# Kernel optimization log

Measured on AMD Instinct MI355X. Metric: run time of the kernel, lower is better.

## Reference

```python
import jax, jax.numpy as jnp
import numpy as np

EPS = 1.1920929e-07  # torch F.rms_norm default eps for fp32
D, NH, NKV, HD = 1024, 16, 4, 64
MLP_MULT, L = 3, 6           # L = num_layers // 2 shared blocks
VS, HS, LS, ROPE_B = 50257, 4096, 30.0, 10000.0
B, S = 2, 2048


def rmsn(x):
    return x * jax.lax.rsqrt(jnp.mean(jnp.square(x), -1, keepdims=True) + EPS)


def rope_tables(s):
    f = 1.0 / ROPE_B ** (jnp.arange(0, HD, 2, dtype=jnp.float32) / HD)
    fr = jnp.outer(jnp.arange(s, dtype=jnp.float32), f)  # [s, HD/2]
    return jnp.cos(fr), jnp.sin(fr)


def rot(x, c, s):
    h = x.shape[-1] // 2
    x1, x2 = x[..., :h], x[..., h:]
    return jnp.concatenate([x1 * c + x2 * s, -x1 * s + x2 * c], -1)


def attn(x, Wq, Wk, Wv, Wo, qg, cos, sin):
    b, s, d = x.shape
    q = (x @ Wq.T).reshape(b, s, NH, HD).swapaxes(1, 2)    # [b,nh,s,hd]
    k = (x @ Wk.T).reshape(b, s, NKV, HD).swapaxes(1, 2)   # [b,nkv,s,hd]
    v = (x @ Wv.T).reshape(b, s, NKV, HD).swapaxes(1, 2)
    q, k = rmsn(q), rmsn(k)                                # QK RMSNorm (no weight)
    c, si = cos[None, None], sin[None, None]
    q, k = rot(q, c, si), rot(k, c, si)
    q = q * qg[None, :, None, None]                        # per-head gate
    g = NH // NKV
    qr = q.reshape(b, NKV, g, s, HD)
    scores = jnp.einsum('bkgqd,bksd->bkgqs', qr, k) / jnp.sqrt(jnp.float32(HD))
    mask = jnp.tril(jnp.ones((s, s), bool))
    scores = jnp.where(mask, scores, -jnp.inf)
    p = jax.nn.softmax(scores, -1)
    y = jnp.einsum('bkgqs,bksd->bkgqd', p, v).reshape(b, NH, s, HD)
    y = y.swapaxes(1, 2).reshape(b, s, d)
    return y @ Wo.T


def mlp(x, Wf, Wo2):
    return jnp.square(jax.nn.relu(x @ Wf.T)) @ Wo2.T       # ReLU^2 MLP


def block(x, x0, p, cos, sin):
    Wq, Wk, Wv, Wo, qg, a_sc, m_sc, rm, Wf, Wo2 = p
    x = rm[0] * x + rm[1] * x0                             # learned residual mix
    x = x + a_sc * attn(rmsn(x), Wq, Wk, Wv, Wo, qg, cos, sin)
    x = x + m_sc * mlp(rmsn(x), Wf, Wo2)
    return x


def setup_inputs() -> dict:
    key = jax.random.key(0)
    ks = jax.random.split(key, 16)
    sd = 0.02
    return {
        'ids': jax.random.randint(ks[0], (B, S), 0, VS, dtype=jnp.int32),
        'y': jax.random.randint(ks[1], (B, S), 0, VS, dtype=jnp.int32),
        'u_emb': jax.random.normal(ks[2], (VS, D // 2), jnp.float32) * 0.02,
        'b_emb': jax.random.normal(ks[3], (HS, D // 2), jnp.float32) * 0.01,
        'Wq': jax.random.normal(ks[4], (L, D, D), jnp.float32) * sd,
        'Wk': jax.random.normal(ks[5], (L, NKV * HD, D), jnp.float32) * sd,
        'Wv': jax.random.normal(ks[6], (L, NKV * HD, D), jnp.float32) * sd,
        'Wo': jax.random.normal(ks[7], (L, D, D), jnp.float32) * sd,
        'qg': jnp.ones((L, NH), jnp.float32),
        'a_scale': jnp.ones((L, D), jnp.float32),
        'm_scale': jnp.ones((L, D), jnp.float32),
        'rm': jnp.stack([jnp.full((L, D), 0.7, jnp.float32), jnp.full((L, D), 0.3, jnp.float32)], 1),
        'Wf': jax.random.normal(ks[8], (L, MLP_MULT * D, D), jnp.float32) * sd,
        'Wo2': jax.random.normal(ks[9], (L, D, MLP_MULT * D), jnp.float32) * sd,
        'sw': jnp.ones((L, D), jnp.float32),
    }


def reference(ids, y, u_emb, b_emb, Wq, Wk, Wv, Wo, qg, a_scale, m_scale, rm, Wf, Wo2, sw):
    b, s = ids.shape
    # BigramHash embedding: (prev_id*VS + id) % HS, computed mod-HS to stay in int32
    pi = jnp.pad(ids[:, :-1], ((0, 0), (1, 0)))
    bi = (((pi % HS) * (VS % HS)) % HS + ids % HS) % HS
    h = jnp.concatenate([u_emb[ids], b_emb[bi]], -1)       # [b,s,D]
    h = rmsn(h)
    cos, sin = rope_tables(s)
    h0, sk = h, []
    for i in range(L):                                     # encoder half
        p = (Wq[i], Wk[i], Wv[i], Wo[i], qg[i], a_scale[i], m_scale[i], rm[i], Wf[i], Wo2[i])
        h = block(h, h0, p, cos, sin)
        sk.append(h)
    for i in range(L):                                     # decoder half (reversed blocks, skips)
        h = h + sw[i] * sk[L - 1 - i]
        j = L - 1 - i
        p = (Wq[j], Wk[j], Wv[j], Wo[j], qg[j], a_scale[j], m_scale[j], rm[j], Wf[j], Wo2[j])
        h = block(h, h0, p, cos, sin)
    h = rmsn(h)
    # tied bigram-hash head: out_weight = [u_emb | zeros]  ->  only first D/2 dims matter
    lg = h.reshape(-1, D)[:, :D // 2] @ u_emb.T            # [b*s, VS]
    lg = LS * jnp.tanh(lg / LS)                            # logit softcap
    logp = jax.nn.log_softmax(lg.astype(jnp.float32), -1)
    yf = y.reshape(-1)
    loss = -jnp.mean(jnp.take_along_axis(logp, yf[:, None], 1)[:, 0])
    return loss
```

## Files before the change

### kernel.cpp

```cpp
#include <hip/hip_runtime.h>
#include <cstdint>
#include <cstddef>

constexpr int   Dm    = 1024;
constexpr int   NHn   = 16;
constexpr int   NKVn  = 4;
constexpr int   HDn   = 64;
constexpr int   Ln    = 6;
constexpr int   Sn    = 2048;
constexpr int   Bn    = 2;
constexpr int   ROWS  = Bn * Sn;
constexpr int   VSn   = 50257;
constexpr int   HSn   = 4096;
constexpr float EPSF  = 1.1920929e-07f;
constexpr int   VCHUNK = 4096;
constexpr int   VPAD   = 50304;
constexpr float LOG2E  = 1.44269504f;

#define DEV __device__ __forceinline__

typedef __attribute__((ext_vector_type(8))) short bf16x8;
typedef __attribute__((ext_vector_type(4))) float f32x4;
using ush = unsigned short;

DEV ush f2bf(float f) {
    unsigned int u = __float_as_uint(f);
    u = (u + 0x7fffu + ((u >> 16) & 1u)) >> 16;
    return (ush)u;
}

DEV float b2f(ush v) {
    return __uint_as_float(((unsigned int)v) << 16);
}

DEV f32x4 mfma16(bf16x8 a, bf16x8 b, f32x4 c) {
    return __builtin_amdgcn_mfma_f32_16x16x32_bf16(a, b, c, 0, 0, 0);
}

DEV void llds16(const ush* g, ush* l) {
    __builtin_amdgcn_global_load_lds(
        (const __attribute__((address_space(1))) void*)g,
        (__attribute__((address_space(3))) void*)l, 16, 0, 0);
}

DEV float block_sum256(float v, float* red) {
#pragma unroll
    for (int off = 32; off; off >>= 1) v += __shfl_xor(v, off);
    __syncthreads();
    if ((threadIdx.x & 63) == 0) red[threadIdx.x >> 6] = v;
    __syncthreads();
    return red[0] + red[1] + red[2] + red[3];
}

DEV float block_max256(float v, float* red) {
#pragma unroll
    for (int off = 32; off; off >>= 1) v = fmaxf(v, __shfl_xor(v, off));
    __syncthreads();
    if ((threadIdx.x & 63) == 0) red[threadIdx.x >> 6] = v;
    __syncthreads();
    return fmaxf(fmaxf(red[0], red[1]), fmaxf(red[2], red[3]));
}

__global__ void rope_kernel(float* __restrict__ cb, float* __restrict__ sb) {
    int idx = blockIdx.x * 256 + threadIdx.x;
    if (idx >= Sn * 32) return;
    int t = idx >> 5, f = idx & 31;
    float freq = powf(10000.f, -(float)f * (1.f / 32.f));
    float ang  = (float)t * freq;
    cb[idx] = cosf(ang);
    sb[idx] = sinf(ang);
}

__global__ void cvt_bf16_kernel(const float* __restrict__ s, ush* __restrict__ d, int n4) {
    int i = blockIdx.x * 256 + threadIdx.x;
    if (i >= n4) return;
    float4 v = *(const float4*)(s + (size_t)i * 4);
    ushort4 o;
    o.x = f2bf(v.x); o.y = f2bf(v.y); o.z = f2bf(v.z); o.w = f2bf(v.w);
    *(ushort4*)(d + (size_t)i * 4) = o;
}

__global__ void zpad_kernel(ush* __restrict__ p, int n) {
    int i = blockIdx.x * 256 + threadIdx.x;
    if (i < n) p[i] = 0;
}

__global__ __launch_bounds__(256)
void embed_kernel(const int* __restrict__ ids, const float* __restrict__ ue,
                  const float* __restrict__ be, float* __restrict__ h,
                  float* __restrict__ h0) {
    __shared__ float red[4];
    int r = blockIdx.x;
    int s = r % Sn;
    int id = ids[r];
    int prev = (s == 0) ? 0 : ids[r - 1];
    int bi = ((prev % HSn) * (VSn % HSn) % HSn + id % HSn) % HSn;
    int tid = threadIdx.x;
    float vals[4];
    float ss = 0.f;
#pragma unroll
    for (int t = 0; t < 4; ++t) {
        int j = tid + t * 256;
        float v = (j < 512) ? ue[(size_t)id * 512 + j]
                            : be[(size_t)bi * 512 + (j - 512)];
        vals[t] = v; ss += v * v;
    }
    ss = block_sum256(ss, red);
    float rinv = rsqrtf(ss * (1.f / Dm) + EPSF);
#pragma unroll
    for (int t = 0; t < 4; ++t) {
        int j = tid + t * 256;
        float v = vals[t] * rinv;
        h [(size_t)r * Dm + j] = v;
        h0[(size_t)r * Dm + j] = v;
    }
}

__global__ __launch_bounds__(256)
void resmix_kernel(float* __restrict__ h, const float* __restrict__ h0,
                   const float* __restrict__ rm0, ush* __restrict__ xnb) {
    __shared__ float red[4];
    int r = blockIdx.x, tid = threadIdx.x;
    const float* rm1 = rm0 + Dm;
    float vals[4]; float ss = 0.f;
#pragma unroll
    for (int t = 0; t < 4; ++t) {
        int j = tid + t * 256;
        size_t o = (size_t)r * Dm + j;
        float v = rm0[j] * h[o] + rm1[j] * h0[o];
        vals[t] = v; ss += v * v;
        h[o] = v;
    }
    ss = block_sum256(ss, red);
    float rinv = rsqrtf(ss * (1.f / Dm) + EPSF);
#pragma unroll
    for (int t = 0; t < 4; ++t)
        xnb[(size_t)r * Dm + tid + t * 256] = f2bf(vals[t] * rinv);
}

__global__ __launch_bounds__(256)
void rmsn_kernel(const float* __restrict__ x, ush* __restrict__ out) {
    __shared__ float red[4];
    int r = blockIdx.x, tid = threadIdx.x;
    float vals[4]; float ss = 0.f;
#pragma unroll
    for (int t = 0; t < 4; ++t) {
        float v = x[(size_t)r * Dm + tid + t * 256];
        vals[t] = v; ss += v * v;
    }
    ss = block_sum256(ss, red);
    float rinv = rsqrtf(ss * (1.f / Dm) + EPSF);
#pragma unroll
    for (int t = 0; t < 4; ++t)
        out[(size_t)r * Dm + tid + t * 256] = f2bf(vals[t] * rinv);
}

__global__ __launch_bounds__(256)
void skipadd_kernel(float* __restrict__ h, const ush* __restrict__ skb,
                    const float* __restrict__ sc) {
    int r = blockIdx.x, tid = threadIdx.x;
#pragma unroll
    for (int t = 0; t < 4; ++t) {
        int j = tid + t * 256;
        size_t o = (size_t)r * Dm + j;
        h[o] = fmaf(sc[j], b2f(skb[o]), h[o]);
    }
}

template<int TM, int MODE>
__global__ __launch_bounds__(256)
void gemm_k(const ush* __restrict__ A, const ush* __restrict__ B,
            ush* __restrict__ C, int M, int N, int K,
            int lda, int ldb, int ldc,
            float* __restrict__ hres, const float* __restrict__ sc,
            ush* __restrict__ dup) {
    __shared__ __align__(16) ush As[TM * 32];
    __shared__ __align__(16) ush Bs[128 * 32];
    const int m0 = blockIdx.x * TM, n0 = blockIdx.y * 128;
    const int tid  = threadIdx.x;
    const int w    = tid >> 6, lane = tid & 63;
    const int l15  = lane & 15, quad = lane >> 4;
    const int wr   = w >> 1, wc = w & 1;
    constexpr int NI = TM / 32;

    const int srow = lane >> 2, sch = lane & 3;
    const ush* Ag;
    ush* AsW;
    if constexpr (TM == 128) {
        Ag  = A + (size_t)(m0 + w * 32 + srow) * lda + sch * 8;
        AsW = As + w * 1024;
    } else {
        Ag  = A + (size_t)(m0 + w * 16 + srow) * lda + sch * 8;
        AsW = As + w * 512;
    }
    const ush* Bg = B + (size_t)(n0 + w * 32 + srow) * ldb + sch * 8;
    ush* BsW = Bs + w * 1024;

    f32x4 acc[NI][4] = {};

    for (int k0 = 0; k0 < K; k0 += 32) {
        __syncthreads();
        llds16(Ag + k0, AsW);
        if constexpr (TM == 128) llds16(Ag + k0 + 16 * lda, AsW + 512);
        llds16(Bg + k0,            BsW);
        llds16(Bg + k0 + 16 * ldb, BsW + 512);
        __syncthreads();
        bf16x8 af[NI], bfv[4];
#pragma unroll
        for (int i = 0; i < NI; ++i)
            af[i] = *(const bf16x8*)&As[(wr * (TM / 2) + i * 16 + l15) * 32 + quad * 8];
#pragma unroll
        for (int j = 0; j < 4; ++j)
            bfv[j] = *(const bf16x8*)&Bs[(wc * 64 + j * 16 + l15) * 32 + quad * 8];
#pragma unroll
        for (int i = 0; i < NI; ++i)
#pragma unroll
            for (int j = 0; j < 4; ++j)
                acc[i][j] = mfma16(af[i], bfv[j], acc[i][j]);
    }

#pragma unroll
    for (int i = 0; i < NI; ++i) {
#pragma unroll
        for (int j = 0; j < 4; ++j) {
            int row = m0 + wr * (TM / 2) + i * 16 + quad * 4;
            int col = n0 + wc * 64 + j * 16 + l15;
#pragma unroll
            for (int r = 0; r < 4; ++r) {
                float v = acc[i][j][r];
                if (MODE == 1) { v = fmaxf(v, 0.f); v = v * v; }
                else if (MODE == 2) {
                    float ax = fabsf(v) * (1.f / 30.f);
                    float e  = __expf(-2.f * ax);
                    float t  = (1.f - e) / (1.f + e);
                    v = copysignf(t * 30.f, v);
                }
                if (MODE == 3) {
                    size_t o = (size_t)(row + r) * ldc + col;
                    float nv = fmaf(sc[col], v, hres[o]);
                    hres[o] = nv;
                    if (dup) dup[o] = f2bf(nv);
                } else {
                    C[(size_t)(row + r) * ldc + col] = f2bf(v);
                }
            }
        }
    }
}

__global__ __launch_bounds__(256)
void qknorm_rope_kernel(const ush* __restrict__ in,
                        ush* __restrict__ qout, ush* __restrict__ kout,
                        const float* __restrict__ cosb, const float* __restrict__ sinb,
                        const float* __restrict__ qg) {
    int idx  = blockIdx.x * 4 + (threadIdx.x >> 6);
    int lane = threadIdx.x & 63;
    int t, hh, in_off;
    ush* outp; int out_ld;
    bool isq = idx < ROWS * NHn;
    if (isq) { t = idx >> 4; hh = idx & 15; in_off = hh * 64; outp = qout; out_ld = 1024; }
    else { int i2 = idx - ROWS * NHn; t = i2 >> 2; hh = i2 & 3; in_off = 1024 + hh * 64; outp = kout; out_ld = 256; }
    int sidx = t % Sn;
    float x = b2f(in[(size_t)t * 1536 + in_off + lane]);
    float ss = x * x;
#pragma unroll
    for (int off = 32; off; off >>= 1) ss += __shfl_xor(ss, off);
    float xn = x * rsqrtf(ss * (1.f / HDn) + EPSF);
    float partner = __shfl_xor(xn, 32);
    int f = lane & 31;
    float c  = cosb[sidx * 32 + f];
    float sv = sinb[sidx * 32 + f];
    float o = (lane < 32) ? fmaf(xn, c, partner * sv)
                          : fmaf(xn, c, -partner * sv);
    if (isq) o *= qg[hh] * (0.125f * LOG2E);
    outp[(size_t)t * out_ld + hh * 64 + lane] = f2bf(o);
}

__global__ __launch_bounds__(256)
void vtrans_kernel(const ush* __restrict__ in, ush* __restrict__ out) {
    __shared__ ush tile[32][33];
    int s0 = blockIdx.x * 32;
    int c0 = blockIdx.y * 32;
    int i = threadIdx.x >> 5;
    int j = threadIdx.x & 31;
#pragma unroll
    for (int k = 0; k < 4; ++k)
        tile[i + k * 8][j] = in[(size_t)(s0 + i + k * 8) * 1536 + 1280 + c0 + j];
    __syncthreads();
#pragma unroll
    for (int k = 0; k < 4; ++k)
        out[(size_t)(c0 + i + k * 8) * (size_t)ROWS + s0 + j] = tile[j][i + k * 8];
}

__global__ __launch_bounds__(256)
void attn_mfma_kernel(const ush* __restrict__ qb,
                      const ush* __restrict__ kb,
                      const ush* __restrict__ vt,
                      ush* __restrict__ ob,
                      const float* __restrict__ qgl) {
    __shared__ __align__(16) ush Ks[64 * 72];
    __shared__ __align__(16) ush Vs[64 * 72];
    __shared__ __align__(16) unsigned int PsD[128 * 36];
    const int tile = 15 - (blockIdx.x & 15);
    const int h    = (blockIdx.x >> 4) & 15;
    const int b    = blockIdx.x >> 8;
    const int kvh  = h >> 2;
    const int w    = threadIdx.x >> 6, lane = threadIdx.x & 63;
    const int l15  = lane & 15, quad = lane >> 4;
    const int q0   = tile * 128;
    const float mfix = 8.f * fabsf(qgl[h]) * LOG2E;

    bf16x8 qf[2][2];
    {
        size_t qr = (size_t)(b * Sn + q0 + w * 32 + l15) * 1024 + h * 64;
        qf[0][0] = *(const bf16x8*)(qb + qr + quad * 8);
        qf[0][1] = *(const bf16x8*)(qb + qr + 32 + quad * 8);
        qf[1][0] = *(const bf16x8*)(qb + qr + 16 * 1024 + quad * 8);
        qf[1][1] = *(const bf16x8*)(qb + qr + 16 * 1024 + 32 + quad * 8);
    }
    f32x4 Oacc[2][4] = {};
    float lsum[2][4] = {{0.f,0.f,0.f,0.f},{0.f,0.f,0.f,0.f}};

    const int rrS = threadIdx.x >> 3, chS = threadIdx.x & 7;
    const size_t kbase = (size_t)(b * Sn) * 256 + kvh * 64;
    const size_t vbase = (size_t)(kvh * 64) * (size_t)ROWS + b * Sn;
    const int nblk = 2 * tile + 2;

    uint4 kr0 = *(const uint4*)(kb + kbase + (size_t)rrS * 256 + chS * 8);
    uint4 kr1 = *(const uint4*)(kb + kbase + (size_t)(rrS + 32) * 256 + chS * 8);
    uint4 vr0 = *(const uint4*)(vt + vbase + (size_t)rrS * ROWS + chS * 8);
    uint4 vr1 = *(const uint4*)(vt + vbase + (size_t)(rrS + 32) * ROWS + chS * 8);

    for (int kb_i = 0; kb_i < nblk; ++kb_i) {
        const int k0 = kb_i * 64;
        __syncthreads();
        *(uint4*)&Ks[rrS * 72 + chS * 8]        = kr0;
        *(uint4*)&Ks[(rrS + 32) * 72 + chS * 8] = kr1;
        *(uint4*)&Vs[rrS * 72 + chS * 8]        = vr0;
        *(uint4*)&Vs[(rrS + 32) * 72 + chS * 8] = vr1;
        __syncthreads();
        if (kb_i + 1 < nblk) {
            int k0n = k0 + 64;
            kr0 = *(const uint4*)(kb + kbase + (size_t)(k0n + rrS) * 256 + chS * 8);
            kr1 = *(const uint4*)(kb + kbase + (size_t)(k0n + rrS + 32) * 256 + chS * 8);
            vr0 = *(const uint4*)(vt + vbase + (size_t)rrS * ROWS + k0n + chS * 8);
            vr1 = *(const uint4*)(vt + vbase + (size_t)(rrS + 32) * ROWS + k0n + chS * 8);
        }

        f32x4 S0[4] = {}, S1[4] = {};
#pragma unroll
        for (int c = 0; c < 4; ++c) {
            bf16x8 kf0 = *(const bf16x8*)&Ks[(c * 16 + l15) * 72 + quad * 8];
            bf16x8 kf1 = *(const bf16x8*)&Ks[(c * 16 + l15) * 72 + 32 + quad * 8];
            S0[c] = mfma16(qf[0][0], kf0, S0[c]);
            S0[c] = mfma16(qf[0][1], kf1, S0[c]);
            S1[c] = mfma16(qf[1][0], kf0, S1[c]);
            S1[c] = mfma16(qf[1][1], kf1, S1[c]);
        }

#pragma unroll
        for (int f = 0; f < 2; ++f) {
            f32x4* S = f ? S1 : S0;
            const int qbF = q0 + w * 32 + f * 16;
            if (k0 + 63 > qbF) {
#pragma unroll
                for (int c = 0; c < 4; ++c) {
                    int key = k0 + c * 16 + l15;
#pragma unroll
                    for (int r = 0; r < 4; ++r)
                        if (key > qbF + quad * 4 + r) S[c][r] = -INFINITY;
                }
            }
#pragma unroll
            for (int c = 0; c < 4; ++c)
#pragma unroll
                for (int r = 0; r < 4; ++r) {
                    float p = exp2f(S[c][r] - mfix);
                    S[c][r] = p;
                    lsum[f][r] += p;
                }
            const int prow = w * 32 + f * 16 + quad * 4;
#pragma unroll
            for (int cp = 0; cp < 2; ++cp)
#pragma unroll
                for (int r = 0; r < 4; ++r) {
                    unsigned int pk = __builtin_amdgcn_perm(
                        __float_as_uint(S[cp + 2][r]), __float_as_uint(S[cp][r]),
                        0x07060302u);
                    PsD[(prow + r) * 36 + cp * 16 + l15] = pk;
                }
        }

#pragma unroll
        for (int f = 0; f < 2; ++f) {
            const int prow = w * 32 + f * 16 + l15;
            unsigned int d[8];
            *(uint4*)&d[0] = *(const uint4*)&PsD[prow * 36 + quad * 8];
            *(uint4*)&d[4] = *(const uint4*)&PsD[prow * 36 + quad * 8 + 4];
            unsigned int lo[4], hi[4];
#pragma unroll
            for (int t = 0; t < 4; ++t) {
                lo[t] = __builtin_amdgcn_perm(d[2 * t + 1], d[2 * t], 0x05040100u);
                hi[t] = __builtin_amdgcn_perm(d[2 * t + 1], d[2 * t], 0x07060302u);
            }
            bf16x8 pf0 = *(const bf16x8*)lo;
            bf16x8 pf1 = *(const bf16x8*)hi;
#pragma unroll
            for (int dt = 0; dt < 4; ++dt) {
                bf16x8 vf0 = *(const bf16x8*)&Vs[(dt * 16 + l15) * 72 + quad * 8];
                bf16x8 vf1 = *(const bf16x8*)&Vs[(dt * 16 + l15) * 72 + 32 + quad * 8];
                Oacc[f][dt] = mfma16(pf0, vf0, Oacc[f][dt]);
                Oacc[f][dt] = mfma16(pf1, vf1, Oacc[f][dt]);
            }
        }
    }

#pragma unroll
    for (int f = 0; f < 2; ++f) {
#pragma unroll
        for (int m = 1; m <= 8; m <<= 1)
#pragma unroll
            for (int r = 0; r < 4; ++r)
                lsum[f][r] += __shfl_xor(lsum[f][r], m);
#pragma unroll
        for (int dt = 0; dt < 4; ++dt)
#pragma unroll
            for (int r = 0; r < 4; ++r) {
                size_t o = (size_t)(b * Sn + q0 + w * 32 + f * 16 + quad * 4 + r) * 1024
                         + h * 64 + dt * 16 + l15;
                ob[o] = f2bf(Oacc[f][dt][r] / lsum[f][r]);
            }
    }
}

__global__ void loss_init_kernel(float* __restrict__ m, float* __restrict__ s,
                                 float* __restrict__ tg) {
    int i = blockIdx.x * 256 + threadIdx.x;
    if (i < ROWS) { m[i] = -INFINITY; s[i] = 0.f; tg[i] = 0.f; }
}

__global__ __launch_bounds__(256)
void chunk_reduce_kernel(const ush* __restrict__ Cc, int Nc, int c0,
                         const int* __restrict__ y, float* __restrict__ m,
                         float* __restrict__ s, float* __restrict__ tg) {
    __shared__ float red[4];
    int r = blockIdx.x, tid = threadIdx.x;
    const ush* row = Cc + (size_t)r * VCHUNK;
    float v[16];
    float mx = -INFINITY;
#pragma unroll
    for (int t = 0; t < 16; ++t) {
        int j = tid + t * 256;
        v[t] = (j < Nc) ? b2f(row[j]) : -INFINITY;
        mx = fmaxf(mx, v[t]);
    }
    mx = block_max256(mx, red);
    float se = 0.f;
#pragma unroll
    for (int t = 0; t < 16; ++t)
        se += __expf(v[t] - mx);
    se = block_sum256(se, red);
    if (tid == 0) {
        float mo = m[r];
        float mn = fmaxf(mo, mx);
        s[r] = s[r] * __expf(mo - mn) + se * __expf(mx - mn);
        m[r] = mn;
        int t = y[r] - c0;
        if (t >= 0 && t < Nc) tg[r] = b2f(row[t]);
    }
}

__global__ __launch_bounds__(256)
void loss_final_kernel(const float* __restrict__ m, const float* __restrict__ s,
                       const float* __restrict__ tg, float* __restrict__ out) {
    __shared__ float red[4];
    float part = 0.f;
    for (int r = threadIdx.x; r < ROWS; r += 256)
        part += m[r] + logf(s[r]) - tg[r];
    part = block_sum256(part, red);
    if (threadIdx.x == 0) out[0] = part * (1.f / ROWS);
}

extern "C" void kernel_launch(void* const* d_in, const int* in_sizes, int n_in,
                              void* d_out, int out_size, void* d_ws, size_t ws_size,
                              hipStream_t stream) {
    const int*   ids = (const int*)d_in[0];
    const int*   yv  = (const int*)d_in[1];
    const float* ue  = (const float*)d_in[2];
    const float* be  = (const float*)d_in[3];
    const float* Wq  = (const float*)d_in[4];
    const float* Wk  = (const float*)d_in[5];
    const float* Wv  = (const float*)d_in[6];
    const float* Wo  = (const float*)d_in[7];
    const float* qg  = (const float*)d_in[8];
    const float* asc = (const float*)d_in[9];
    const float* msc = (const float*)d_in[10];
    const float* rm  = (const float*)d_in[11];
    const float* Wf  = (const float*)d_in[12];
    const float* Wo2 = (const float*)d_in[13];
    const float* sw  = (const float*)d_in[14];
    (void)in_sizes; (void)n_in; (void)out_size; (void)ws_size;

    char* wsb = (char*)d_ws;
    size_t off = 0;
    auto alloc = [&](size_t bytes) {
        void* p = (void*)(wsb + off);
        off += ((bytes + 255) & ~size_t(255));
        return p;
    };
    float* h    = (float*)alloc((size_t)ROWS * Dm * 4);
    float* h0   = (float*)alloc((size_t)ROWS * Dm * 4);
    float* cosb = (float*)alloc((size_t)Sn * 32 * 4);
    float* sinb = (float*)alloc((size_t)Sn * 32 * 4);
    float* mrow = (float*)alloc(ROWS * 4);
    float* srow = (float*)alloc(ROWS * 4);
    float* tgv  = (float*)alloc(ROWS * 4);
    ush* skb  = (ush*)alloc((size_t)Ln * ROWS * Dm * 2);
    ush* xnb  = (ush*)alloc((size_t)ROWS * Dm * 2);
    ush* qkvb = (ush*)alloc((size_t)ROWS * 1536 * 2);
    ush* qbf  = (ush*)alloc((size_t)ROWS * Dm * 2);
    ush* kbf  = (ush*)alloc((size_t)ROWS * 256 * 2);
    ush* vtb  = (ush*)alloc((size_t)256 * ROWS * 2);
    ush* attb = (ush*)alloc((size_t)ROWS * Dm * 2);
    ush* hidb = (ush*)alloc((size_t)ROWS * 3 * Dm * 2);
    ush* wall = (ush*)alloc((size_t)Ln * 8704 * 1024 * 2);
    ush* ueb  = (ush*)alloc((size_t)VPAD * 512 * 2);
    ush* chunk = skb;

    auto cvt = [&](const float* s, ush* d, size_t n) {
        int n4 = (int)(n / 4);
        cvt_bf16_kernel<<<(n4 + 255) / 256, 256, 0, stream>>>(s, d, n4);
    };

    for (int l = 0; l < Ln; ++l) {
        ush* wl = wall + (size_t)l * 8704 * 1024;
        cvt(Wq + (size_t)l * Dm * Dm,      wl,              (size_t)Dm * Dm);
        cvt(Wk + (size_t)l * 256 * Dm,     wl + 1024 * Dm,  (size_t)256 * Dm);
        cvt(Wv + (size_t)l * 256 * Dm,     wl + 1280 * Dm,  (size_t)256 * Dm);
        cvt(Wo + (size_t)l * Dm * Dm,      wl + 1536 * Dm,  (size_t)Dm * Dm);
        cvt(Wf + (size_t)l * 3 * Dm * Dm,  wl + 2560 * Dm,  (size_t)3 * Dm * Dm);
        cvt(Wo2 + (size_t)l * 3 * Dm * Dm, wl + 5632 * Dm,  (size_t)3 * Dm * Dm);
    }
    cvt(ue, ueb, (size_t)VSn * 512);
    zpad_kernel<<<((VPAD - VSn) * 512 + 255) / 256, 256, 0, stream>>>(
        ueb + (size_t)VSn * 512, (VPAD - VSn) * 512);

    rope_kernel<<<(Sn * 32 + 255) / 256, 256, 0, stream>>>(cosb, sinb);
    embed_kernel<<<ROWS, 256, 0, stream>>>(ids, ue, be, h, h0);

    auto run_block = [&](int l, ush* dup) {
        ush* wl    = wall + (size_t)l * 8704 * 1024;
        ush* wqkvb = wl;
        ush* wob   = wl + (size_t)1536 * 1024;
        ush* wfb   = wl + (size_t)2560 * 1024;
        ush* wo2b  = wl + (size_t)5632 * 1024;

        resmix_kernel<<<ROWS, 256, 0, stream>>>(h, h0, rm + (size_t)l * 2 * Dm, xnb);
        gemm_k<64, 0><<<dim3(ROWS / 64, 1536 / 128), 256, 0, stream>>>(
            xnb, wqkvb, qkvb, ROWS, 1536, Dm, Dm, Dm, 1536, nullptr, nullptr, nullptr);
        qknorm_rope_kernel<<<ROWS * (NHn + NKVn) / 4, 256, 0, stream>>>(
            qkvb, qbf, kbf, cosb, sinb, qg + (size_t)l * NHn);
        vtrans_kernel<<<dim3(ROWS / 32, 8), 256, 0, stream>>>(qkvb, vtb);
        attn_mfma_kernel<<<Bn * NHn * 16, 256, 0, stream>>>(
            qbf, kbf, vtb, attb, qg + (size_t)l * NHn);
        gemm_k<64, 3><<<dim3(ROWS / 64, Dm / 128), 256, 0, stream>>>(
            attb, wob, nullptr, ROWS, Dm, Dm, Dm, Dm, Dm,
            h, asc + (size_t)l * Dm, nullptr);
        rmsn_kernel<<<ROWS, 256, 0, stream>>>(h, xnb);
        gemm_k<128, 1><<<dim3(ROWS / 128, 3 * Dm / 128), 256, 0, stream>>>(
            xnb, wfb, hidb, ROWS, 3 * Dm, Dm, Dm, Dm, 3 * Dm, nullptr, nullptr, nullptr);
        gemm_k<64, 3><<<dim3(ROWS / 64, Dm / 128), 256, 0, stream>>>(
            hidb, wo2b, nullptr, ROWS, Dm, 3 * Dm, 3 * Dm, 3 * Dm, Dm,
            h, msc + (size_t)l * Dm, dup);
    };

    for (int l = 0; l < Ln; ++l)
        run_block(l, skb + (size_t)l * ROWS * Dm);
    for (int i = 0; i < Ln; ++i) {
        int j = Ln - 1 - i;
        skipadd_kernel<<<ROWS, 256, 0, stream>>>(h, skb + (size_t)j * ROWS * Dm,
                                                 sw + (size_t)i * Dm);
        run_block(j, nullptr);
    }

    rmsn_kernel<<<ROWS, 256, 0, stream>>>(h, xnb);
    loss_init_kernel<<<(ROWS + 255) / 256, 256, 0, stream>>>(mrow, srow, tgv);
    for (int c0 = 0; c0 < VSn; c0 += VCHUNK) {
        int Nc = (VSn - c0 < VCHUNK) ? (VSn - c0) : VCHUNK;
        int Ng = (VPAD - c0 < VCHUNK) ? (VPAD - c0) : VCHUNK;
        gemm_k<128, 2><<<dim3(ROWS / 128, Ng / 128), 256, 0, stream>>>(
            xnb, ueb + (size_t)c0 * 512, chunk, ROWS, Ng, 512, Dm, 512, VCHUNK,
            nullptr, nullptr, nullptr);
        chunk_reduce_kernel<<<ROWS, 256, 0, stream>>>(chunk, Nc, c0, yv, mrow, srow, tgv);
    }
    loss_final_kernel<<<1, 256, 0, stream>>>(mrow, srow, tgv, (float*)d_out);
}
```

Before: 4.390 ms.

## Split causal attention along keys into chunks and fuse skip-add into resmix

```diff
diff --git a/kernel.cpp b/kernel.cpp
--- a/kernel.cpp
+++ b/kernel.cpp
@@ -116,9 +116,11 @@
     }
 }
 
+template<bool SKIP>
 __global__ __launch_bounds__(256)
 void resmix_kernel(float* __restrict__ h, const float* __restrict__ h0,
-                   const float* __restrict__ rm0, ush* __restrict__ xnb) {
+                   const float* __restrict__ rm0, ush* __restrict__ xnb,
+                   const ush* __restrict__ skb, const float* __restrict__ sw) {
     __shared__ float red[4];
     int r = blockIdx.x, tid = threadIdx.x;
     const float* rm1 = rm0 + Dm;
@@ -127,7 +129,9 @@
     for (int t = 0; t < 4; ++t) {
         int j = tid + t * 256;
         size_t o = (size_t)r * Dm + j;
-        float v = rm0[j] * h[o] + rm1[j] * h0[o];
+        float base = h[o];
+        if (SKIP) base = fmaf(sw[j], b2f(skb[o]), base);
+        float v = rm0[j] * base + rm1[j] * h0[o];
         vals[t] = v; ss += v * v;
         h[o] = v;
     }
@@ -153,18 +157,6 @@
 #pragma unroll
     for (int t = 0; t < 4; ++t)
         out[(size_t)r * Dm + tid + t * 256] = f2bf(vals[t] * rinv);
-}
-
-__global__ __launch_bounds__(256)
-void skipadd_kernel(float* __restrict__ h, const ush* __restrict__ skb,
-                    const float* __restrict__ sc) {
-    int r = blockIdx.x, tid = threadIdx.x;
-#pragma unroll
-    for (int t = 0; t < 4; ++t) {
-        int j = tid + t * 256;
-        size_t o = (size_t)r * Dm + j;
-        h[o] = fmaf(sc[j], b2f(skb[o]), h[o]);
-    }
 }
 
 template<int TM, int MODE>
@@ -296,18 +288,28 @@
 void attn_mfma_kernel(const ush* __restrict__ qb,
                       const ush* __restrict__ kb,
                       const ush* __restrict__ vt,
-                      ush* __restrict__ ob,
+                      ush* __restrict__ opart,
+                      float* __restrict__ lpart,
                       const float* __restrict__ qgl) {
     __shared__ __align__(16) ush Ks[64 * 72];
     __shared__ __align__(16) ush Vs[64 * 72];
     __shared__ __align__(16) unsigned int PsD[128 * 36];
-    const int tile = 15 - (blockIdx.x & 15);
-    const int h    = (blockIdx.x >> 4) & 15;
-    const int b    = blockIdx.x >> 8;
+    const int pair = blockIdx.x % 40;
+    const int bh   = blockIdx.x / 40;
+    const int h    = bh & 15;
+    const int b    = bh >> 4;
+    const int g    = (pair >= 24) ? 3 : (pair >= 12) ? 2 : (pair >= 4) ? 1 : 0;
+    const int off_p = pair - 2 * g * (g + 1);
+    const int t    = 4 * g + off_p / (g + 1);
+    const int c    = off_p % (g + 1);
     const int kvh  = h >> 2;
     const int w    = threadIdx.x >> 6, lane = threadIdx.x & 63;
     const int l15  = lane & 15, quad = lane >> 4;
-    const int q0   = tile * 128;
+    const int q0   = t * 128;
+    const int k_lo = c * 512;
+    const int k_hi_full = (t + 1) * 128;
+    const int k_hi = (k_lo + 512 < k_hi_full) ? (k_lo + 512) : k_hi_full;
+    const int nblk = (k_hi - k_lo) >> 6;
     const float mfix = 8.f * fabsf(qgl[h]) * LOG2E;
 
     bf16x8 qf[2][2];
@@ -324,15 +326,14 @@
     const int rrS = threadIdx.x >> 3, chS = threadIdx.x & 7;
     const size_t kbase = (size_t)(b * Sn) * 256 + kvh * 64;
     const size_t vbase = (size_t)(kvh * 64) * (size_t)ROWS + b * Sn;
-    const int nblk = 2 * tile + 2;
-
-    uint4 kr0 = *(const uint4*)(kb + kbase + (size_t)rrS * 256 + chS * 8);
-    uint4 kr1 = *(const uint4*)(kb + kbase + (size_t)(rrS + 32) * 256 + chS * 8);
-    uint4 vr0 = *(const uint4*)(vt + vbase + (size_t)rrS * ROWS + chS * 8);
-    uint4 vr1 = *(const uint4*)(vt + vbase + (size_t)(rrS + 32) * ROWS + chS * 8);
+
+    uint4 kr0 = *(const uint4*)(kb + kbase + (size_t)(k_lo + rrS) * 256 + chS * 8);
+    uint4 kr1 = *(const uint4*)(kb + kbase + (size_t)(k_lo + rrS + 32) * 256 + chS * 8);
+    uint4 vr0 = *(const uint4*)(vt + vbase + (size_t)rrS * ROWS + k_lo + chS * 8);
+    uint4 vr1 = *(const uint4*)(vt + vbase + (size_t)(rrS + 32) * ROWS + k_lo + chS * 8);
 
     for (int kb_i = 0; kb_i < nblk; ++kb_i) {
-        const int k0 = kb_i * 64;
+        const int k0 = k_lo + kb_i * 64;
         __syncthreads();
         *(uint4*)&Ks[rrS * 72 + chS * 8]        = kr0;
         *(uint4*)&Ks[(rrS + 32) * 72 + chS * 8] = kr1;
@@ -349,13 +350,13 @@
 
         f32x4 S0[4] = {}, S1[4] = {};
 #pragma unroll
-        for (int c = 0; c < 4; ++c) {
-            bf16x8 kf0 = *(const bf16x8*)&Ks[(c * 16 + l15) * 72 + quad * 8];
-            bf16x8 kf1 = *(const bf16x8*)&Ks[(c * 16 + l15) * 72 + 32 + quad * 8];
-            S0[c] = mfma16(qf[0][0], kf0, S0[c]);
-            S0[c] = mfma16(qf[0][1], kf1, S0[c]);
-            S1[c] = mfma16(qf[1][0], kf0, S1[c]);
-            S1[c] = mfma16(qf[1][1], kf1, S1[c]);
+        for (int cc = 0; cc < 4; ++cc) {
+            bf16x8 kf0 = *(const bf16x8*)&Ks[(cc * 16 + l15) * 72 + quad * 8];
+            bf16x8 kf1 = *(const bf16x8*)&Ks[(cc * 16 + l15) * 72 + 32 + quad * 8];
+            S0[cc] = mfma16(qf[0][0], kf0, S0[cc]);
+            S0[cc] = mfma16(qf[0][1], kf1, S0[cc]);
+            S1[cc] = mfma16(qf[1][0], kf0, S1[cc]);
+            S1[cc] = mfma16(qf[1][1], kf1, S1[cc]);
         }
 
 #pragma unroll
@@ -364,19 +365,19 @@
             const int qbF = q0 + w * 32 + f * 16;
             if (k0 + 63 > qbF) {
 #pragma unroll
-                for (int c = 0; c < 4; ++c) {
-                    int key = k0 + c * 16 + l15;
+                for (int cc = 0; cc < 4; ++cc) {
+                    int key = k0 + cc * 16 + l15;
 #pragma unroll
                     for (int r = 0; r < 4; ++r)
-                        if (key > qbF + quad * 4 + r) S[c][r] = -INFINITY;
+                        if (key > qbF + quad * 4 + r) S[cc][r] = -INFINITY;
                 }
             }
 #pragma unroll
-            for (int c = 0; c < 4; ++c)
+            for (int cc = 0; cc < 4; ++cc)
 #pragma unroll
                 for (int r = 0; r < 4; ++r) {
-                    float p = exp2f(S[c][r] - mfix);
-                    S[c][r] = p;
+                    float p = exp2f(S[cc][r] - mfix);
+                    S[cc][r] = p;
                     lsum[f][r] += p;
                 }
             const int prow = w * 32 + f * 16 + quad * 4;
@@ -399,9 +400,9 @@
             *(uint4*)&d[4] = *(const uint4*)&PsD[prow * 36 + quad * 8 + 4];
             unsigned int lo[4], hi[4];
 #pragma unroll
-            for (int t = 0; t < 4; ++t) {
-                lo[t] = __builtin_amdgcn_perm(d[2 * t + 1], d[2 * t], 0x05040100u);
-                hi[t] = __builtin_amdgcn_perm(d[2 * t + 1], d[2 * t], 0x07060302u);
+            for (int tt = 0; tt < 4; ++tt) {
+                lo[tt] = __builtin_amdgcn_perm(d[2 * tt + 1], d[2 * tt], 0x05040100u);
+                hi[tt] = __builtin_amdgcn_perm(d[2 * tt + 1], d[2 * tt], 0x07060302u);
             }
             bf16x8 pf0 = *(const bf16x8*)lo;
             bf16x8 pf1 = *(const bf16x8*)hi;
@@ -423,14 +424,37 @@
             for (int r = 0; r < 4; ++r)
                 lsum[f][r] += __shfl_xor(lsum[f][r], m);
 #pragma unroll
-        for (int dt = 0; dt < 4; ++dt)
-#pragma unroll
-            for (int r = 0; r < 4; ++r) {
-                size_t o = (size_t)(b * Sn + q0 + w * 32 + f * 16 + quad * 4 + r) * 1024
-                         + h * 64 + dt * 16 + l15;
-                ob[o] = f2bf(Oacc[f][dt][r] / lsum[f][r]);
-            }
-    }
+        for (int r = 0; r < 4; ++r) {
+            int token = b * Sn + q0 + w * 32 + f * 16 + quad * 4 + r;
+            if (l15 == 0)
+                lpart[((size_t)c * ROWS + token) * NHn + h] = lsum[f][r];
+#pragma unroll
+            for (int dt = 0; dt < 4; ++dt)
+                opart[((size_t)c * ROWS + token) * 1024 + h * 64 + dt * 16 + l15]
+                    = f2bf(Oacc[f][dt][r]);
+        }
+    }
+}
+
+__global__ __launch_bounds__(256)
+void attn_combine_kernel(const ush* __restrict__ opart,
+                         const float* __restrict__ lpart,
+                         ush* __restrict__ attb) {
+    int token = blockIdx.x;
+    int j = threadIdx.x * 4;
+    int head = j >> 6;
+    int nc = ((token % Sn) >> 9) + 1;
+    float a0 = 0.f, a1 = 0.f, a2 = 0.f, a3 = 0.f, l = 0.f;
+    for (int cc = 0; cc < nc; ++cc) {
+        ushort4 o4 = *(const ushort4*)(opart + ((size_t)cc * ROWS + token) * 1024 + j);
+        a0 += b2f(o4.x); a1 += b2f(o4.y); a2 += b2f(o4.z); a3 += b2f(o4.w);
+        l  += lpart[((size_t)cc * ROWS + token) * NHn + head];
+    }
+    float rin = 1.f / l;
+    ushort4 out;
+    out.x = f2bf(a0 * rin); out.y = f2bf(a1 * rin);
+    out.z = f2bf(a2 * rin); out.w = f2bf(a3 * rin);
+    *(ushort4*)(attb + (size_t)token * 1024 + j) = out;
 }
 
 __global__ void loss_init_kernel(float* __restrict__ m, float* __restrict__ s,
@@ -515,14 +539,16 @@
     float* mrow = (float*)alloc(ROWS * 4);
     float* srow = (float*)alloc(ROWS * 4);
     float* tgv  = (float*)alloc(ROWS * 4);
+    float* lpart= (float*)alloc((size_t)4 * ROWS * NHn * 4);
     ush* skb  = (ush*)alloc((size_t)Ln * ROWS * Dm * 2);
     ush* xnb  = (ush*)alloc((size_t)ROWS * Dm * 2);
     ush* qkvb = (ush*)alloc((size_t)ROWS * 1536 * 2);
+    ush* hidb = (ush*)alloc((size_t)ROWS * 3 * Dm * 2);
+    ush* opart = qkvb;
     ush* qbf  = (ush*)alloc((size_t)ROWS * Dm * 2);
     ush* kbf  = (ush*)alloc((size_t)ROWS * 256 * 2);
     ush* vtb  = (ush*)alloc((size_t)256 * ROWS * 2);
     ush* attb = (ush*)alloc((size_t)ROWS * Dm * 2);
-    ush* hidb = (ush*)alloc((size_t)ROWS * 3 * Dm * 2);
     ush* wall = (ush*)alloc((size_t)Ln * 8704 * 1024 * 2);
     ush* ueb  = (ush*)alloc((size_t)VPAD * 512 * 2);
     ush* chunk = skb;
@@ -548,21 +574,27 @@
     rope_kernel<<<(Sn * 32 + 255) / 256, 256, 0, stream>>>(cosb, sinb);
     embed_kernel<<<ROWS, 256, 0, stream>>>(ids, ue, be, h, h0);
 
-    auto run_block = [&](int l, ush* dup) {
+    auto run_block = [&](int l, ush* dup, const ush* skip, const float* swv) {
         ush* wl    = wall + (size_t)l * 8704 * 1024;
         ush* wqkvb = wl;
         ush* wob   = wl + (size_t)1536 * 1024;
         ush* wfb   = wl + (size_t)2560 * 1024;
         ush* wo2b  = wl + (size_t)5632 * 1024;
 
-        resmix_kernel<<<ROWS, 256, 0, stream>>>(h, h0, rm + (size_t)l * 2 * Dm, xnb);
+        if (skip)
+            resmix_kernel<true><<<ROWS, 256, 0, stream>>>(
+                h, h0, rm + (size_t)l * 2 * Dm, xnb, skip, swv);
+        else
+            resmix_kernel<false><<<ROWS, 256, 0, stream>>>(
+                h, h0, rm + (size_t)l * 2 * Dm, xnb, nullptr, nullptr);
         gemm_k<64, 0><<<dim3(ROWS / 64, 1536 / 128), 256, 0, stream>>>(
             xnb, wqkvb, qkvb, ROWS, 1536, Dm, Dm, Dm, 1536, nullptr, nullptr, nullptr);
         qknorm_rope_kernel<<<ROWS * (NHn + NKVn) / 4, 256, 0, stream>>>(
             qkvb, qbf, kbf, cosb, sinb, qg + (size_t)l * NHn);
         vtrans_kernel<<<dim3(ROWS / 32, 8), 256, 0, stream>>>(qkvb, vtb);
-        attn_mfma_kernel<<<Bn * NHn * 16, 256, 0, stream>>>(
-            qbf, kbf, vtb, attb, qg + (size_t)l * NHn);
+        attn_mfma_kernel<<<Bn * NHn * 40, 256, 0, stream>>>(
+            qbf, kbf, vtb, opart, lpart, qg + (size_t)l * NHn);
+        attn_combine_kernel<<<ROWS, 256, 0, stream>>>(opart, lpart, attb);
         gemm_k<64, 3><<<dim3(ROWS / 64, Dm / 128), 256, 0, stream>>>(
             attb, wob, nullptr, ROWS, Dm, Dm, Dm, Dm, Dm,
             h, asc + (size_t)l * Dm, nullptr);
@@ -575,12 +607,10 @@
     };
 
     for (int l = 0; l < Ln; ++l)
-        run_block(l, skb + (size_t)l * ROWS * Dm);
+        run_block(l, skb + (size_t)l * ROWS * Dm, nullptr, nullptr);
     for (int i = 0; i < Ln; ++i) {
         int j = Ln - 1 - i;
-        skipadd_kernel<<<ROWS, 256, 0, stream>>>(h, skb + (size_t)j * ROWS * Dm,
-                                                 sw + (size_t)i * Dm);
-        run_block(j, nullptr);
+        run_block(j, nullptr, skb + (size_t)j * ROWS * Dm, sw + (size_t)i * Dm);
     }
 
     rmsn_kernel<<<ROWS, 256, 0, stream>>>(h, xnb);
```

Result: faster. 4.210 ms (-4.1%).
